# Kernel tuning notes

Hardware: AMD Instinct MI355X
Metric: run time of the kernel (lower is better)

The kernel has to match this reference:

```python
import jax, jax.numpy as jnp
import numpy as np

SDR_SIZE = 2048
CAPACITY = 131072
N_ACTIVE = 40
CONTENT_DIM = 384
THRESHOLD = 0.3
N_PLANTED = 64  # rows made similar to the query so top-k hits pass the threshold


def setup_inputs() -> dict:
    key = jax.random.key(0)
    k1, k2, k3, k4 = jax.random.split(key, 4)
    p = N_ACTIVE / SDR_SIZE
    query_sdr = (jax.random.uniform(k1, (SDR_SIZE,)) < p).astype(jnp.float32)
    sdr_bank = (jax.random.uniform(k2, (CAPACITY, SDR_SIZE)) < p).astype(jnp.float32)
    # plant near-duplicates of the query so retrieval has matches above threshold
    noise = (jax.random.uniform(k4, (N_PLANTED, SDR_SIZE)) < 0.1).astype(jnp.float32)
    planted = jnp.clip(query_sdr[None, :] * (1.0 - noise) + noise * sdr_bank[:N_PLANTED], 0.0, 1.0)
    sdr_bank = sdr_bank.at[:N_PLANTED].set(planted)
    content_bank = jax.random.normal(k3, (CAPACITY, CONTENT_DIM), dtype=jnp.float32)
    valid_mask = jnp.ones((CAPACITY,), dtype=bool)  # buffer is full (count == capacity)
    return {
        "query_sdr": query_sdr,
        "sdr_bank": sdr_bank,
        "content_bank": content_bank,
        "valid_mask": valid_mask,
        "top_k": 32,
    }


def reference(query_sdr, sdr_bank, content_bank, valid_mask, top_k):
    # overlap = number of shared active bits  -> [capacity]
    overlap = sdr_bank @ query_sdr
    similarity = overlap / N_ACTIVE
    similarity = jnp.where(valid_mask, similarity, -jnp.inf)
    top_sim, top_idx = jax.lax.top_k(similarity, top_k)
    # torch version filters by boolean mask (dynamic shape); here we keep
    # fixed shape [top_k] and zero out entries below threshold instead.
    keep = top_sim >= THRESHOLD
    contents = content_bank[top_idx]                      # [top_k, content_dim]
    contents = jnp.where(keep[:, None], contents, 0.0)
    top_sim = jnp.where(keep, top_sim, 0.0)
    return contents, top_sim
```

## Files before the change

kernel.cpp:

```cpp
#include <hip/hip_runtime.h>
#include <stdint.h>

#define SDR_SIZE   2048
#define CAPACITY   131072
#define TOPK       32
#define CDIM       384
#define RPW        8


__global__ void k_prep(const float* __restrict__ q, int* __restrict__ w) {
    __shared__ int s_cnt;
    __shared__ int s_act[256];
    if (threadIdx.x == 0) s_cnt = 0;
    __syncthreads();
    for (int j = threadIdx.x; j < SDR_SIZE; j += 256) {
        if (q[j] != 0.0f) {
            int p = atomicAdd(&s_cnt, 1);
            if (p < 256) s_act[p] = j;
        }
    }
    __syncthreads();
    if (threadIdx.x == 0) {
        int n = s_cnt < 128 ? s_cnt : 128;
        for (int i = 1; i < n; i++) {
            int v = s_act[i]; int k = i - 1;
            while (k >= 0 && s_act[k] > v) { s_act[k + 1] = s_act[k]; k--; }
            s_act[k + 1] = v;
        }
        w[0] = n;
        w[192] = 0;
        for (int i = 0; i < n; i++) w[4 + i] = s_act[i];
    }
}

__global__ __launch_bounds__(256) void k_overlap(const float* __restrict__ bank,
                                                 const int* __restrict__ mask,
                                                 int* __restrict__ w, int cap) {
    const int wave = (blockIdx.x * 256 + (int)threadIdx.x) >> 6;
    const int lane = threadIdx.x & 63;
    const int sub  = lane & 7;
    const int row  = wave * RPW + (lane >> 3);
    const int nact = w[0];
    const float* rp = bank + (size_t)row * SDR_SIZE;
    int ov = 0;
    for (int idx = sub; idx < nact; idx += 8) {
        int c = w[4 + idx];
        ov += (rp[c] != 0.0f) ? 1 : 0;
    }
    ov += __shfl_xor(ov, 1);
    ov += __shfl_xor(ov, 2);
    ov += __shfl_xor(ov, 4);
    if (sub == 0) {
        float sim = (float)ov / 40.0f;
        if (mask[row] != 0 && sim >= 0.3f) {
            int p = atomicAdd(&w[192], 1);
            if (p < cap) w[256 + p] = (ov << 17) | (131071 - row);
        }
    }
}

__global__ void k_select(const float* __restrict__ content,
                         const int* __restrict__ w,
                         float* __restrict__ out, int cap) {
    __shared__ unsigned int s_top[TOPK];
    int t = threadIdx.x;
    int m = w[192];
    if (m > cap) m = cap;
    int kcount = (m < TOPK) ? m : TOPK;
    if (t < 64) {
        unsigned int prev = 0xFFFFFFFFu;
        for (int s = 0; s < kcount; s++) {
            unsigned int best = 0;
            for (int i = t; i < m; i += 64) {
                unsigned int k = (unsigned int)w[256 + i];
                if (k < prev && k > best) best = k;
            }
            for (int off = 1; off < 64; off <<= 1) {
                unsigned int o = (unsigned int)__shfl_xor((int)best, off);
                best = o > best ? o : best;
            }
            prev = best;
            if (t == 0) s_top[s] = best;
        }
    }
    __syncthreads();
    for (int i = t; i < TOPK * CDIM; i += 256) {
        int s = i / CDIM, d = i - s * CDIM;
        float val = 0.0f;
        if (s < kcount) {
            int idx = CAPACITY - 1 - (int)(s_top[s] & 0x1FFFFu);
            val = content[(size_t)idx * CDIM + d];
        }
        out[i] = val;
    }
    if (t < TOPK) {
        float sv = 0.0f;
        if (t < kcount) sv = (float)(s_top[t] >> 17) / 40.0f;
        out[TOPK * CDIM + t] = sv;
    }
}

extern "C" void kernel_launch(void* const* d_in, const int* in_sizes, int n_in,
                              void* d_out, int out_size, void* d_ws, size_t ws_size,
                              hipStream_t stream) {
    const float* query   = (const float*)d_in[0];
    const float* bank    = (const float*)d_in[1];
    const float* content = (const float*)d_in[2];
    const int* mask      = (const int*)d_in[3];
    float* out = (float*)d_out;
    int* w = (int*)d_ws;

    size_t words = ws_size / 4;
    int cap = (int)((words > 256) ? (words - 256) : 0);
    if (cap > 65536) cap = 65536;

    k_prep<<<1, 256, 0, stream>>>(query, w);
    k_overlap<<<CAPACITY / (RPW * 4), 256, 0, stream>>>(bank, mask, w, cap);
    k_select<<<1, 256, 0, stream>>>(content, w, out, cap);
}
```

Baseline: 1.357 ms.

## Replace sparse gather overlap with dense coalesced dot product per row

After: 1.411 ms. 4.0% more time.

```diff
diff --git a/kernel.cpp b/kernel.cpp
--- a/kernel.cpp
+++ b/kernel.cpp
@@ -5,56 +5,29 @@
 #define CAPACITY   131072
 #define TOPK       32
 #define CDIM       384
-#define RPW        8
 
 
-__global__ void k_prep(const float* __restrict__ q, int* __restrict__ w) {
-    __shared__ int s_cnt;
-    __shared__ int s_act[256];
-    if (threadIdx.x == 0) s_cnt = 0;
-    __syncthreads();
-    for (int j = threadIdx.x; j < SDR_SIZE; j += 256) {
-        if (q[j] != 0.0f) {
-            int p = atomicAdd(&s_cnt, 1);
-            if (p < 256) s_act[p] = j;
-        }
-    }
-    __syncthreads();
-    if (threadIdx.x == 0) {
-        int n = s_cnt < 128 ? s_cnt : 128;
-        for (int i = 1; i < n; i++) {
-            int v = s_act[i]; int k = i - 1;
-            while (k >= 0 && s_act[k] > v) { s_act[k + 1] = s_act[k]; k--; }
-            s_act[k + 1] = v;
-        }
-        w[0] = n;
-        w[192] = 0;
-        for (int i = 0; i < n; i++) w[4 + i] = s_act[i];
-    }
-}
-
 __global__ __launch_bounds__(256) void k_overlap(const float* __restrict__ bank,
+                                                 const float* __restrict__ q,
                                                  const int* __restrict__ mask,
                                                  int* __restrict__ w, int cap) {
     const int wave = (blockIdx.x * 256 + (int)threadIdx.x) >> 6;
     const int lane = threadIdx.x & 63;
-    const int sub  = lane & 7;
-    const int row  = wave * RPW + (lane >> 3);
-    const int nact = w[0];
-    const float* rp = bank + (size_t)row * SDR_SIZE;
-    int ov = 0;
-    for (int idx = sub; idx < nact; idx += 8) {
-        int c = w[4 + idx];
-        ov += (rp[c] != 0.0f) ? 1 : 0;
+    const float4* rp = (const float4*)(bank + (size_t)wave * SDR_SIZE);
+    const float4* qp = (const float4*)q;
+    float acc = 0.0f;
+    #pragma unroll
+    for (int i = 0; i < 8; i++) {
+        float4 v  = rp[lane + i * 64];
+        float4 qq = qp[lane + i * 64];
+        acc += v.x * qq.x + v.y * qq.y + v.z * qq.z + v.w * qq.w;
     }
-    ov += __shfl_xor(ov, 1);
-    ov += __shfl_xor(ov, 2);
-    ov += __shfl_xor(ov, 4);
-    if (sub == 0) {
-        float sim = (float)ov / 40.0f;
-        if (mask[row] != 0 && sim >= 0.3f) {
+    for (int off = 1; off < 64; off <<= 1) acc += __shfl_xor(acc, off);
+    if (lane == 0) {
+        int ov = (int)acc;
+        if (mask[wave] != 0 && ov >= 12) {
             int p = atomicAdd(&w[192], 1);
-            if (p < cap) w[256 + p] = (ov << 17) | (131071 - row);
+            if (p < cap) w[256 + p] = (ov << 17) | (131071 - wave);
         }
     }
 }
@@ -114,7 +87,7 @@
     int cap = (int)((words > 256) ? (words - 256) : 0);
     if (cap > 65536) cap = 65536;
 
-    k_prep<<<1, 256, 0, stream>>>(query, w);
-    k_overlap<<<CAPACITY / (RPW * 4), 256, 0, stream>>>(bank, mask, w, cap);
+    hipMemsetAsync((void*)(w + 192), 0, 4, stream);
+    k_overlap<<<CAPACITY / 4, 256, 0, stream>>>(bank, query, mask, w, cap);
     k_select<<<1, 256, 0, stream>>>(content, w, out, cap);
 }
```
